# Kernel optimization log

Hardware: AMD Instinct MI355X
Metric: run time of the kernel (lower is better)

The kernel has to match this reference:

```python
import jax, jax.numpy as jnp
import numpy as np

D_MODEL = 1024
N_HEADS = 16
D_K = D_MODEL // N_HEADS


def setup_inputs() -> dict:
    key = jax.random.key(0)
    ks = jax.random.split(key, 9)
    B, S = 4, 2048
    scale = 1.0 / np.sqrt(D_MODEL)
    x = jax.random.normal(ks[0], (B, S, D_MODEL), dtype=jnp.float32)
    # Linear params: weight [out,in] (torch convention), bias [out]
    wq = jax.random.uniform(ks[1], (D_MODEL, D_MODEL), jnp.float32, -scale, scale)
    bq = jax.random.uniform(ks[2], (D_MODEL,), jnp.float32, -scale, scale)
    wk = jax.random.uniform(ks[3], (D_MODEL, D_MODEL), jnp.float32, -scale, scale)
    bk = jax.random.uniform(ks[4], (D_MODEL,), jnp.float32, -scale, scale)
    wv = jax.random.uniform(ks[5], (D_MODEL, D_MODEL), jnp.float32, -scale, scale)
    bv = jax.random.uniform(ks[6], (D_MODEL,), jnp.float32, -scale, scale)
    wo = jax.random.uniform(ks[7], (D_MODEL, D_MODEL), jnp.float32, -scale, scale)
    bo = jax.random.uniform(ks[8], (D_MODEL,), jnp.float32, -scale, scale)
    return {"x": x, "wq": wq, "bq": bq, "wk": wk, "bk": bk,
            "wv": wv, "bv": bv, "wo": wo, "bo": bo}


def reference(x, wq, bq, wk, bk, wv, bv, wo, bo):
    B, S, _ = x.shape
    # QKV projections (torch Linear: x @ W^T + b)
    q = x @ wq.T + bq
    k = x @ wk.T + bk
    v = x @ wv.T + bv
    # [B, H, S, D_K]
    q = q.reshape(B, S, N_HEADS, D_K).transpose(0, 2, 1, 3)
    k = k.reshape(B, S, N_HEADS, D_K).transpose(0, 2, 1, 3)
    v = v.reshape(B, S, N_HEADS, D_K).transpose(0, 2, 1, 3)
    scores = jnp.einsum('bhqd,bhkd->bhqk', q, k) / jnp.sqrt(jnp.float32(D_K))
    attn = jax.nn.softmax(scores, axis=-1)
    out = jnp.einsum('bhqk,bhkd->bhqd', attn, v)
    out = out.transpose(0, 2, 1, 3).reshape(B, S, D_MODEL)
    return out @ wo.T + bo
```

## Files before the change

kernel.cpp:

```cpp
#include <hip/hip_runtime.h>

#define DMODEL 1024
#define NHEADS 16
#define DK 64
#define BATCH 4
#define SEQ 2048
#define MROWS (BATCH * SEQ)
#define NT 16

typedef __attribute__((ext_vector_type(8))) short bf16x8;
typedef __attribute__((ext_vector_type(8))) unsigned short u16x8;
typedef __attribute__((ext_vector_type(4))) unsigned short u16x4;
typedef __attribute__((ext_vector_type(4))) float f32x4;
typedef __attribute__((ext_vector_type(16))) float f32x16;
typedef __attribute__((ext_vector_type(2))) unsigned int u32x2;
typedef __attribute__((ext_vector_type(4))) unsigned int u32x4;

using gld_gptr = const __attribute__((address_space(1))) unsigned int*;
using gld_lptr = __attribute__((address_space(3))) unsigned int*;

#define QSCALE 0.18033688011112042f

__device__ inline unsigned short f32_bf16(float f) {
    unsigned int u = __float_as_uint(f);
    u += 0x7FFFu + ((u >> 16) & 1u);
    return (unsigned short)(u >> 16);
}

__device__ inline unsigned int cvtpk_bf16(float a, float b) {
    unsigned int r;
    asm("v_cvt_pk_bf16_f32 %0, %1, %2" : "=v"(r) : "v"(a), "v"(b));
    return r;
}

__device__ inline f32x16 fz16() {
    f32x16 v;
#pragma unroll
    for (int i = 0; i < 16; ++i) v[i] = 0.f;
    return v;
}

struct Conv5 {
    const float* s[5];
    unsigned short* d[5];
};

__global__ __launch_bounds__(256) void conv5_kernel(Conv5 c) {
    int bx = blockIdx.x;
    int which, idx;
    if (bx < 4096) { which = 0; idx = bx; }
    else { which = 1 + ((bx - 4096) >> 9); idx = (bx - 4096) & 511; }
    int i = idx * 256 + threadIdx.x;
    const float4* s = (const float4*)(c.s[which] + (size_t)i * 8);
    float4 a = s[0], b = s[1];
    u16x8 o;
    o[0] = f32_bf16(a.x); o[1] = f32_bf16(a.y); o[2] = f32_bf16(a.z); o[3] = f32_bf16(a.w);
    o[4] = f32_bf16(b.x); o[5] = f32_bf16(b.y); o[6] = f32_bf16(b.z); o[7] = f32_bf16(b.w);
    *(u16x8*)(c.d[which] + (size_t)i * 8) = o;
}


__device__ __forceinline__ void stage_half(const unsigned short* mat, int row0, int step,
                                           char* lds_half, int tid) {
#pragma unroll
    for (int rnd = 0; rnd < 2; ++rnd) {
        int rl = rnd * 64 + (tid >> 3);
        int c16 = (tid & 7) ^ (rl & 7);
        const unsigned short* g = mat + (size_t)(row0 + rl) * DMODEL + step * 64 + c16 * 8;
        __builtin_amdgcn_global_load_lds((gld_gptr)g,
            (gld_lptr)(lds_half + rnd * 8192 + (tid >> 6) * 1024), 16, 0, 0);
    }
}

__device__ __forceinline__ bf16x8 lds_frag(const char* base, int row, int kk, int l) {
    int kb = kk * 64 + (l >> 4) * 16;
    return *(const bf16x8*)(base + row * 128 + (kb ^ ((row & 7) << 4)));
}

template <int QP>
__device__ __forceinline__ void phase_reads(const char* Ab, const char* Bb,
                                            bf16x8 (&breg)[4][2], bf16x8 (&areg)[2][2],
                                            int wm, int wn, int l) {
    int l15 = l & 15;
    if constexpr (QP == 0) {
#pragma unroll
        for (int nt = 0; nt < 4; ++nt)
#pragma unroll
            for (int kk = 0; kk < 2; ++kk)
                breg[nt][kk] = lds_frag(Bb, wn * 64 + nt * 16 + l15, kk, l);
    }
#pragma unroll
    for (int j = 0; j < 2; ++j)
#pragma unroll
        for (int kk = 0; kk < 2; ++kk)
            areg[j][kk] = lds_frag(Ab, wm * 128 + (QP * 2 + j) * 16 + l15, kk, l);
}

template <int QP>
__device__ __forceinline__ void phase_mfma(bf16x8 (&areg)[2][2], bf16x8 (&breg)[4][2],
                                           f32x4 (&acc)[8][4]) {
    __builtin_amdgcn_s_setprio(1);
#pragma unroll
    for (int j = 0; j < 2; ++j)
#pragma unroll
        for (int nt = 0; nt < 4; ++nt) {
            acc[QP * 2 + j][nt] = __builtin_amdgcn_mfma_f32_16x16x32_bf16(
                areg[j][0], breg[nt][0], acc[QP * 2 + j][nt], 0, 0, 0);
            acc[QP * 2 + j][nt] = __builtin_amdgcn_mfma_f32_16x16x32_bf16(
                areg[j][1], breg[nt][1], acc[QP * 2 + j][nt], 0, 0, 0);
        }
    __builtin_amdgcn_s_setprio(0);
}

#define GBAR() __builtin_amdgcn_s_barrier()
#define VMC4() asm volatile("s_waitcnt vmcnt(4)" ::: "memory")

template <bool F32OUT>
__device__ __forceinline__ void gemm_core(const unsigned short* __restrict__ Am,
                                          const unsigned short* __restrict__ Bm,
                                          const float* __restrict__ bias, void* Cv,
                                          float scl, int m0, int n0) {
    __shared__ __align__(16) char lds[131072];
    char* A0 = lds;
    char* B0 = lds + 32768;
    char* A1 = lds + 65536;
    char* B1 = lds + 98304;

    int tid = threadIdx.x, l = tid & 63, w = tid >> 6;
    int wm = w >> 2, wn = w & 3;

    f32x4 acc[8][4];
#pragma unroll
    for (int i = 0; i < 8; ++i)
#pragma unroll
        for (int j = 0; j < 4; ++j) acc[i][j] = (f32x4){0.f, 0.f, 0.f, 0.f};

    stage_half(Am, m0,       0, A0,         tid);
    stage_half(Am, m0 + 128, 0, A0 + 16384, tid);
    stage_half(Bm, n0,       0, B0,         tid);
    stage_half(Bm, n0 + 128, 0, B0 + 16384, tid);
    stage_half(Bm, n0,       1, B1,         tid);
    stage_half(Bm, n0 + 128, 1, B1 + 16384, tid);
    VMC4();
    GBAR();

    bf16x8 breg[4][2];
    for (int i = 0; i < NT / 2; ++i) {
        int E = 2 * i;
        bf16x8 areg[2][2];
        phase_reads<0>(A0, B0, breg, areg, wm, wn, l);
        stage_half(Am, m0,       (E + 1) & 15, A1, tid);
        GBAR(); phase_mfma<0>(areg, breg, acc); GBAR();

        phase_reads<1>(A0, B0, breg, areg, wm, wn, l);
        stage_half(Am, m0 + 128, (E + 1) & 15, A1 + 16384, tid);
        GBAR(); phase_mfma<1>(areg, breg, acc); GBAR();

        phase_reads<2>(A0, B0, breg, areg, wm, wn, l);
        stage_half(Bm, n0,       (E + 2) & 15, B0, tid);
        GBAR(); phase_mfma<2>(areg, breg, acc); GBAR();

        phase_reads<3>(A0, B0, breg, areg, wm, wn, l);
        stage_half(Bm, n0 + 128, (E + 2) & 15, B0 + 16384, tid);
        GBAR(); phase_mfma<3>(areg, breg, acc);
        VMC4();
        GBAR();

        phase_reads<0>(A1, B1, breg, areg, wm, wn, l);
        stage_half(Am, m0,       (E + 2) & 15, A0, tid);
        GBAR(); phase_mfma<0>(areg, breg, acc); GBAR();

        phase_reads<1>(A1, B1, breg, areg, wm, wn, l);
        stage_half(Am, m0 + 128, (E + 2) & 15, A0 + 16384, tid);
        GBAR(); phase_mfma<1>(areg, breg, acc); GBAR();

        phase_reads<2>(A1, B1, breg, areg, wm, wn, l);
        stage_half(Bm, n0,       (E + 3) & 15, B1, tid);
        GBAR(); phase_mfma<2>(areg, breg, acc); GBAR();

        phase_reads<3>(A1, B1, breg, areg, wm, wn, l);
        stage_half(Bm, n0 + 128, (E + 3) & 15, B1 + 16384, tid);
        GBAR(); phase_mfma<3>(areg, breg, acc);
        VMC4();
        GBAR();
    }

    int lm = l >> 4, ln = l & 15;
#pragma unroll
    for (int nt = 0; nt < 4; ++nt) {
        int col = n0 + wn * 64 + nt * 16 + ln;
        float bv = bias[col];
#pragma unroll
        for (int mt = 0; mt < 8; ++mt)
#pragma unroll
            for (int r = 0; r < 4; ++r) {
                int row = m0 + wm * 128 + mt * 16 + lm * 4 + r;
                float v = (acc[mt][nt][r] + bv) * scl;
                if constexpr (F32OUT)
                    ((float*)Cv)[(size_t)row * DMODEL + col] = v;
                else
                    ((unsigned short*)Cv)[(size_t)row * DMODEL + col] = f32_bf16(v);
            }
    }
}

struct QkvPtrs {
    const unsigned short* w[3];
    const float* b[3];
    unsigned short* c[3];
    float scale[3];
};

__global__ __launch_bounds__(512, 2) void gemm_qkv8(const unsigned short* __restrict__ A, QkvPtrs p) {
    int sel = blockIdx.y >> 2;
    int n0 = (blockIdx.y & 3) * 256;
    int m0 = blockIdx.x * 256;
    gemm_core<false>(A, p.w[sel], p.b[sel], p.c[sel], p.scale[sel], m0, n0);
}

__global__ __launch_bounds__(512, 2) void gemm_out8(const unsigned short* __restrict__ A,
                                                    const unsigned short* __restrict__ B,
                                                    const float* __restrict__ bias,
                                                    float* __restrict__ C) {
    gemm_core<true>(A, B, bias, C, 1.0f, blockIdx.x * 256, blockIdx.y * 256);
}

#define BUILD_PW(dst, pv, o)                                                        \
    {                                                                               \
        unsigned int wa_ = cvtpk_bf16(pv[(o) + 0], pv[(o) + 1]);                    \
        unsigned int wb_ = cvtpk_bf16(pv[(o) + 2], pv[(o) + 3]);                    \
        unsigned int wc_ = cvtpk_bf16(pv[(o) + 4], pv[(o) + 5]);                    \
        unsigned int wd_ = cvtpk_bf16(pv[(o) + 6], pv[(o) + 7]);                    \
        u32x2 ra_ = __builtin_amdgcn_permlane32_swap(wa_, wc_, false, false);       \
        u32x2 rb_ = __builtin_amdgcn_permlane32_swap(wb_, wd_, false, false);       \
        dst = (u32x4){ra_[0], rb_[0], ra_[1], rb_[1]};                              \
    }

__global__ __launch_bounds__(256, 3) void attn_kernel(const unsigned short* __restrict__ Q,
                                                      const unsigned short* __restrict__ Km,
                                                      const unsigned short* __restrict__ Vm,
                                                      unsigned short* __restrict__ O) {
    __shared__ unsigned short Klds[64 * 64];
    __shared__ unsigned short Vt[64 * 64];

    int flat = blockIdx.y * gridDim.x + blockIdx.x;
    int xcd = flat & 7, idx = flat >> 3;
    int bh = xcd * 8 + (idx & 7);
    int qt = idx >> 3;
    int b = bh >> 4, h = bh & 15;
    int tid = threadIdx.x, l = tid & 63, w = tid >> 6;
    int lq = l & 31, hf = l >> 5;
    const size_t base = ((size_t)b * SEQ) * DMODEL + (size_t)h * DK;
    const unsigned short* qp = Q + base;
    const unsigned short* kp = Km + base;
    const unsigned short* vp = Vm + base;
    int qrow = qt * 128 + w * 32 + lq;

    bf16x8 qf[4];
#pragma unroll
    for (int ks = 0; ks < 4; ++ks)
        qf[ks] = *(const bf16x8*)&qp[(size_t)qrow * DMODEL + ks * 16 + hf * 8];

    f32x16 accO[2];
    accO[0] = fz16(); accO[1] = fz16();
    float l_r = 0.f;

    for (int kt = 0; kt < SEQ / 64; ++kt) {
        __syncthreads();
#pragma unroll
        for (int i = 0; i < 2; ++i) {
            int chunk = w + i * 4;
            int row = chunk * 8 + (l >> 3);
            int srccol = (l & 7) ^ (l >> 3);
            const unsigned short* g = kp + (size_t)(kt * 64 + row) * DMODEL + srccol * 8;
            __builtin_amdgcn_global_load_lds((gld_gptr)g, (gld_lptr)(Klds + chunk * 512), 16, 0, 0);
        }
        {
            int kvp = (tid & 31) * 2;
            int d0 = (tid >> 5) * 8;
            bf16x8 va = *(const bf16x8*)&vp[(size_t)(kt * 64 + kvp) * DMODEL + d0];
            bf16x8 vb = *(const bf16x8*)&vp[(size_t)(kt * 64 + kvp + 1) * DMODEL + d0];
#pragma unroll
            for (int j = 0; j < 8; ++j) {
                int d = d0 + j;
                unsigned int val = ((unsigned int)(unsigned short)va[j]) |
                                   (((unsigned int)(unsigned short)vb[j]) << 16);
                int byt = d * 128 + (((kvp >> 3) ^ (d & 7)) << 4) + (kvp & 7) * 2;
                *(unsigned int*)((char*)Vt + byt) = val;
            }
        }
        __syncthreads();

        f32x16 s0 = fz16(), s1 = fz16();
#pragma unroll
        for (int ks = 0; ks < 4; ++ks) {
            int col16 = ks * 2 + hf;
            bf16x8 kf0 = *(const bf16x8*)((const char*)Klds + lq * 128 + ((col16 ^ (lq & 7)) << 4));
            bf16x8 kf1 = *(const bf16x8*)((const char*)Klds + (lq + 32) * 128 + ((col16 ^ (lq & 7)) << 4));
            s0 = __builtin_amdgcn_mfma_f32_32x32x16_bf16(kf0, qf[ks], s0, 0, 0, 0);
            s1 = __builtin_amdgcn_mfma_f32_32x32x16_bf16(kf1, qf[ks], s1, 0, 0, 0);
        }

        float rs = 0.f;
#pragma unroll
        for (int r = 0; r < 16; ++r) { s0[r] = __builtin_amdgcn_exp2f(s0[r]); rs += s0[r]; }
#pragma unroll
        for (int r = 0; r < 16; ++r) { s1[r] = __builtin_amdgcn_exp2f(s1[r]); rs += s1[r]; }
        rs += __shfl_xor(rs, 32);
        l_r += rs;

        u32x4 pw[4];
        BUILD_PW(pw[0], s0, 0);
        BUILD_PW(pw[1], s0, 8);
        BUILD_PW(pw[2], s1, 0);
        BUILD_PW(pw[3], s1, 8);

#pragma unroll
        for (int ks = 0; ks < 4; ++ks) {
            bf16x8 pf = *(bf16x8*)&pw[ks];
            int col16 = ks * 2 + hf;
#pragma unroll
            for (int db = 0; db < 2; ++db) {
                int d = db * 32 + lq;
                bf16x8 vf = *(const bf16x8*)((const char*)Vt + d * 128 + ((col16 ^ (d & 7)) << 4));
                accO[db] = __builtin_amdgcn_mfma_f32_32x32x16_bf16(vf, pf, accO[db], 0, 0, 0);
            }
        }
    }

    float inv = 1.0f / l_r;
    unsigned short* op = O + base + (size_t)qrow * DMODEL;
#pragma unroll
    for (int db = 0; db < 2; ++db)
#pragma unroll
        for (int rg = 0; rg < 4; ++rg) {
            int dbase = db * 32 + rg * 8 + hf * 4;
            u16x4 ov;
#pragma unroll
            for (int j = 0; j < 4; ++j) ov[j] = f32_bf16(accO[db][rg * 4 + j] * inv);
            *(u16x4*)&op[dbase] = ov;
        }
}

extern "C" void kernel_launch(void* const* d_in, const int* in_sizes, int n_in,
                              void* d_out, int out_size, void* d_ws, size_t ws_size,
                              hipStream_t stream) {
    (void)in_sizes; (void)n_in; (void)out_size; (void)ws_size;
    const float* x  = (const float*)d_in[0];
    const float* wq = (const float*)d_in[1];
    const float* bq = (const float*)d_in[2];
    const float* wk = (const float*)d_in[3];
    const float* bk = (const float*)d_in[4];
    const float* wv = (const float*)d_in[5];
    const float* bv = (const float*)d_in[6];
    const float* wo = (const float*)d_in[7];
    const float* bo = (const float*)d_in[8];
    float* out = (float*)d_out;
    char* ws = (char*)d_ws;

    unsigned short* xb  = (unsigned short*)(ws);
    unsigned short* wqb = (unsigned short*)(ws + (16ull << 20));
    unsigned short* wkb = (unsigned short*)(ws + (18ull << 20));
    unsigned short* wvb = (unsigned short*)(ws + (20ull << 20));
    unsigned short* wob = (unsigned short*)(ws + (22ull << 20));
    unsigned short* qb  = (unsigned short*)(ws + (24ull << 20));
    unsigned short* kb  = (unsigned short*)(ws + (40ull << 20));
    unsigned short* vb  = (unsigned short*)(ws + (56ull << 20));
    unsigned short* ob  = xb;

    Conv5 cv;
    cv.s[0] = x;  cv.d[0] = xb;
    cv.s[1] = wq; cv.d[1] = wqb;
    cv.s[2] = wk; cv.d[2] = wkb;
    cv.s[3] = wv; cv.d[3] = wvb;
    cv.s[4] = wo; cv.d[4] = wob;
    conv5_kernel<<<4096 + 4 * 512, 256, 0, stream>>>(cv);

    QkvPtrs p;
    p.w[0] = wqb; p.w[1] = wkb; p.w[2] = wvb;
    p.b[0] = bq;  p.b[1] = bk;  p.b[2] = bv;
    p.c[0] = qb;  p.c[1] = kb;  p.c[2] = vb;
    p.scale[0] = QSCALE; p.scale[1] = 1.0f; p.scale[2] = 1.0f;
    gemm_qkv8<<<dim3(32, 12), 512, 0, stream>>>(xb, p);

    attn_kernel<<<dim3(16, 64), 256, 0, stream>>>(qb, kb, vb, ob);

    gemm_out8<<<dim3(32, 4), 512, 0, stream>>>(ob, wob, bo, out);
}
```

Measured before the change: 200.5 us.

## Double-buffer K/V tiles and double Q rows per wave in attention

The attention kernel now double-buffers the K and V shared-memory tiles, prefetching the next tile while MFMAs run on the current one. This replaces two __syncthreads per tile with a single barrier. Each wave now handles 64 query rows instead of 32, so every K/V fragment read from LDS feeds twice as many MFMAs, and the grid is halved to match. The changes also add s_setprio around the MFMA blocks and lower launch bounds occupancy to 2, trading occupancy and more registers for better reuse and latency hiding.

Result: faster. 188.9 us (-5.8%).

```diff
diff --git a/kernel.cpp b/kernel.cpp
--- a/kernel.cpp
+++ b/kernel.cpp
@@ -59,7 +59,6 @@
     *(u16x8*)(c.d[which] + (size_t)i * 8) = o;
 }
 
-
 __device__ __forceinline__ void stage_half(const unsigned short* mat, int row0, int step,
                                            char* lds_half, int tid) {
 #pragma unroll
@@ -236,12 +235,47 @@
         dst = (u32x4){ra_[0], rb_[0], ra_[1], rb_[1]};                              \
     }
 
-__global__ __launch_bounds__(256, 3) void attn_kernel(const unsigned short* __restrict__ Q,
+#define ABAR() asm volatile("s_barrier" ::: "memory")
+#define AVMC0() asm volatile("s_waitcnt vmcnt(0)" ::: "memory")
+
+__device__ __forceinline__ void stage_k(const unsigned short* kp, int kt,
+                                        unsigned short* kbuf, int l, int w) {
+#pragma unroll
+    for (int i = 0; i < 2; ++i) {
+        int chunk = w + i * 4;
+        int srccol = (l & 7) ^ (l >> 3);
+        const unsigned short* g = kp + (size_t)(kt * 64 + chunk * 8 + (l >> 3)) * DMODEL + srccol * 8;
+        __builtin_amdgcn_global_load_lds((gld_gptr)g, (gld_lptr)(kbuf + chunk * 512), 16, 0, 0);
+    }
+}
+
+__device__ __forceinline__ void load_v(const unsigned short* vp, int kt, int tid,
+                                       bf16x8& va, bf16x8& vb) {
+    int kvp = (tid & 31) * 2;
+    int d0 = (tid >> 5) * 8;
+    va = *(const bf16x8*)&vp[(size_t)(kt * 64 + kvp) * DMODEL + d0];
+    vb = *(const bf16x8*)&vp[(size_t)(kt * 64 + kvp + 1) * DMODEL + d0];
+}
+
+__device__ __forceinline__ void write_v(unsigned short* vbuf, int tid, bf16x8 va, bf16x8 vb) {
+    int kvp = (tid & 31) * 2;
+    int d0 = (tid >> 5) * 8;
+#pragma unroll
+    for (int j = 0; j < 8; ++j) {
+        int d = d0 + j;
+        unsigned int val = ((unsigned int)(unsigned short)va[j]) |
+                           (((unsigned int)(unsigned short)vb[j]) << 16);
+        int byt = d * 128 + (((kvp >> 3) ^ (d & 7)) << 4) + (kvp & 7) * 2;
+        *(unsigned int*)((char*)vbuf + byt) = val;
+    }
+}
+
+__global__ __launch_bounds__(256, 2) void attn_kernel(const unsigned short* __restrict__ Q,
                                                       const unsigned short* __restrict__ Km,
                                                       const unsigned short* __restrict__ Vm,
                                                       unsigned short* __restrict__ O) {
-    __shared__ unsigned short Klds[64 * 64];
-    __shared__ unsigned short Vt[64 * 64];
+    __shared__ unsigned short Klds[2][64 * 64];
+    __shared__ unsigned short Vt[2][64 * 64];
 
     int flat = blockIdx.y * gridDim.x + blockIdx.x;
     int xcd = flat & 7, idx = flat >> 3;
@@ -254,92 +288,103 @@
     const unsigned short* qp = Q + base;
     const unsigned short* kp = Km + base;
     const unsigned short* vp = Vm + base;
-    int qrow = qt * 128 + w * 32 + lq;
-
-    bf16x8 qf[4];
-#pragma unroll
-    for (int ks = 0; ks < 4; ++ks)
-        qf[ks] = *(const bf16x8*)&qp[(size_t)qrow * DMODEL + ks * 16 + hf * 8];
-
-    f32x16 accO[2];
-    accO[0] = fz16(); accO[1] = fz16();
-    float l_r = 0.f;
+    int q0 = qt * 256 + w * 64;
+
+    bf16x8 qf[2][4];
+#pragma unroll
+    for (int sb = 0; sb < 2; ++sb)
+#pragma unroll
+        for (int ks = 0; ks < 4; ++ks)
+            qf[sb][ks] = *(const bf16x8*)&qp[(size_t)(q0 + sb * 32 + lq) * DMODEL + ks * 16 + hf * 8];
+
+    f32x16 accO[2][2];
+    accO[0][0] = fz16(); accO[0][1] = fz16(); accO[1][0] = fz16(); accO[1][1] = fz16();
+    float l_r[2] = {0.f, 0.f};
+
+    bf16x8 va, vb;
+    stage_k(kp, 0, Klds[0], l, w);
+    load_v(vp, 0, tid, va, vb);
+    AVMC0();
+    write_v(Vt[0], tid, va, vb);
+    ABAR();
 
     for (int kt = 0; kt < SEQ / 64; ++kt) {
-        __syncthreads();
-#pragma unroll
-        for (int i = 0; i < 2; ++i) {
-            int chunk = w + i * 4;
-            int row = chunk * 8 + (l >> 3);
-            int srccol = (l & 7) ^ (l >> 3);
-            const unsigned short* g = kp + (size_t)(kt * 64 + row) * DMODEL + srccol * 8;
-            __builtin_amdgcn_global_load_lds((gld_gptr)g, (gld_lptr)(Klds + chunk * 512), 16, 0, 0);
-        }
-        {
-            int kvp = (tid & 31) * 2;
-            int d0 = (tid >> 5) * 8;
-            bf16x8 va = *(const bf16x8*)&vp[(size_t)(kt * 64 + kvp) * DMODEL + d0];
-            bf16x8 vb = *(const bf16x8*)&vp[(size_t)(kt * 64 + kvp + 1) * DMODEL + d0];
-#pragma unroll
-            for (int j = 0; j < 8; ++j) {
-                int d = d0 + j;
-                unsigned int val = ((unsigned int)(unsigned short)va[j]) |
-                                   (((unsigned int)(unsigned short)vb[j]) << 16);
-                int byt = d * 128 + (((kvp >> 3) ^ (d & 7)) << 4) + (kvp & 7) * 2;
-                *(unsigned int*)((char*)Vt + byt) = val;
-            }
-        }
-        __syncthreads();
-
-        f32x16 s0 = fz16(), s1 = fz16();
+        int cur = kt & 1, nxt = cur ^ 1;
+        bool pre = (kt + 1 < SEQ / 64);
+        if (pre) {
+            stage_k(kp, kt + 1, Klds[nxt], l, w);
+            load_v(vp, kt + 1, tid, va, vb);
+        }
+
+        f32x16 s[2][2];
+        s[0][0] = fz16(); s[0][1] = fz16(); s[1][0] = fz16(); s[1][1] = fz16();
+        __builtin_amdgcn_s_setprio(1);
 #pragma unroll
         for (int ks = 0; ks < 4; ++ks) {
             int col16 = ks * 2 + hf;
-            bf16x8 kf0 = *(const bf16x8*)((const char*)Klds + lq * 128 + ((col16 ^ (lq & 7)) << 4));
-            bf16x8 kf1 = *(const bf16x8*)((const char*)Klds + (lq + 32) * 128 + ((col16 ^ (lq & 7)) << 4));
-            s0 = __builtin_amdgcn_mfma_f32_32x32x16_bf16(kf0, qf[ks], s0, 0, 0, 0);
-            s1 = __builtin_amdgcn_mfma_f32_32x32x16_bf16(kf1, qf[ks], s1, 0, 0, 0);
-        }
-
-        float rs = 0.f;
-#pragma unroll
-        for (int r = 0; r < 16; ++r) { s0[r] = __builtin_amdgcn_exp2f(s0[r]); rs += s0[r]; }
-#pragma unroll
-        for (int r = 0; r < 16; ++r) { s1[r] = __builtin_amdgcn_exp2f(s1[r]); rs += s1[r]; }
-        rs += __shfl_xor(rs, 32);
-        l_r += rs;
-
-        u32x4 pw[4];
-        BUILD_PW(pw[0], s0, 0);
-        BUILD_PW(pw[1], s0, 8);
-        BUILD_PW(pw[2], s1, 0);
-        BUILD_PW(pw[3], s1, 8);
-
+            bf16x8 kf0 = *(const bf16x8*)((const char*)Klds[cur] + lq * 128 + ((col16 ^ (lq & 7)) << 4));
+            bf16x8 kf1 = *(const bf16x8*)((const char*)Klds[cur] + (lq + 32) * 128 + ((col16 ^ (lq & 7)) << 4));
+            s[0][0] = __builtin_amdgcn_mfma_f32_32x32x16_bf16(kf0, qf[0][ks], s[0][0], 0, 0, 0);
+            s[0][1] = __builtin_amdgcn_mfma_f32_32x32x16_bf16(kf1, qf[0][ks], s[0][1], 0, 0, 0);
+            s[1][0] = __builtin_amdgcn_mfma_f32_32x32x16_bf16(kf0, qf[1][ks], s[1][0], 0, 0, 0);
+            s[1][1] = __builtin_amdgcn_mfma_f32_32x32x16_bf16(kf1, qf[1][ks], s[1][1], 0, 0, 0);
+        }
+        __builtin_amdgcn_s_setprio(0);
+
+        u32x4 pw[2][4];
+#pragma unroll
+        for (int sb = 0; sb < 2; ++sb) {
+            float rs = 0.f;
+#pragma unroll
+            for (int r = 0; r < 16; ++r) { s[sb][0][r] = __builtin_amdgcn_exp2f(s[sb][0][r]); rs += s[sb][0][r]; }
+#pragma unroll
+            for (int r = 0; r < 16; ++r) { s[sb][1][r] = __builtin_amdgcn_exp2f(s[sb][1][r]); rs += s[sb][1][r]; }
+            rs += __shfl_xor(rs, 32);
+            l_r[sb] += rs;
+            BUILD_PW(pw[sb][0], s[sb][0], 0);
+            BUILD_PW(pw[sb][1], s[sb][0], 8);
+            BUILD_PW(pw[sb][2], s[sb][1], 0);
+            BUILD_PW(pw[sb][3], s[sb][1], 8);
+        }
+
+        __builtin_amdgcn_s_setprio(1);
 #pragma unroll
         for (int ks = 0; ks < 4; ++ks) {
-            bf16x8 pf = *(bf16x8*)&pw[ks];
             int col16 = ks * 2 + hf;
-#pragma unroll
-            for (int db = 0; db < 2; ++db) {
-                int d = db * 32 + lq;
-                bf16x8 vf = *(const bf16x8*)((const char*)Vt + d * 128 + ((col16 ^ (d & 7)) << 4));
-                accO[db] = __builtin_amdgcn_mfma_f32_32x32x16_bf16(vf, pf, accO[db], 0, 0, 0);
+            int d1 = 32 + lq;
+            bf16x8 vf0 = *(const bf16x8*)((const char*)Vt[cur] + lq * 128 + ((col16 ^ (lq & 7)) << 4));
+            bf16x8 vf1 = *(const bf16x8*)((const char*)Vt[cur] + d1 * 128 + ((col16 ^ (d1 & 7)) << 4));
+            bf16x8 pf0 = *(bf16x8*)&pw[0][ks];
+            bf16x8 pf1 = *(bf16x8*)&pw[1][ks];
+            accO[0][0] = __builtin_amdgcn_mfma_f32_32x32x16_bf16(vf0, pf0, accO[0][0], 0, 0, 0);
+            accO[0][1] = __builtin_amdgcn_mfma_f32_32x32x16_bf16(vf1, pf0, accO[0][1], 0, 0, 0);
+            accO[1][0] = __builtin_amdgcn_mfma_f32_32x32x16_bf16(vf0, pf1, accO[1][0], 0, 0, 0);
+            accO[1][1] = __builtin_amdgcn_mfma_f32_32x32x16_bf16(vf1, pf1, accO[1][1], 0, 0, 0);
+        }
+        __builtin_amdgcn_s_setprio(0);
+
+        if (pre) {
+            AVMC0();
+            write_v(Vt[nxt], tid, va, vb);
+        }
+        ABAR();
+    }
+
+#pragma unroll
+    for (int sb = 0; sb < 2; ++sb) {
+        float inv = 1.0f / l_r[sb];
+        unsigned short* op = O + base + (size_t)(q0 + sb * 32 + lq) * DMODEL;
+#pragma unroll
+        for (int db = 0; db < 2; ++db)
+#pragma unroll
+            for (int rg = 0; rg < 4; ++rg) {
+                int dbase = db * 32 + rg * 8 + hf * 4;
+                u16x4 ov;
+#pragma unroll
+                for (int j = 0; j < 4; ++j) ov[j] = f32_bf16(accO[sb][db][rg * 4 + j] * inv);
+                *(u16x4*)&op[dbase] = ov;
             }
-        }
-    }
-
-    float inv = 1.0f / l_r;
-    unsigned short* op = O + base + (size_t)qrow * DMODEL;
-#pragma unroll
-    for (int db = 0; db < 2; ++db)
-#pragma unroll
-        for (int rg = 0; rg < 4; ++rg) {
-            int dbase = db * 32 + rg * 8 + hf * 4;
-            u16x4 ov;
-#pragma unroll
-            for (int j = 0; j < 4; ++j) ov[j] = f32_bf16(accO[db][rg * 4 + j] * inv);
-            *(u16x4*)&op[dbase] = ov;
-        }
+    }
 }
 
 extern "C" void kernel_launch(void* const* d_in, const int* in_sizes, int n_in,
@@ -383,7 +428,7 @@
     p.scale[0] = QSCALE; p.scale[1] = 1.0f; p.scale[2] = 1.0f;
     gemm_qkv8<<<dim3(32, 12), 512, 0, stream>>>(xb, p);
 
-    attn_kernel<<<dim3(16, 64), 256, 0, stream>>>(qb, kb, vb, ob);
+    attn_kernel<<<dim3(8, 64), 256, 0, stream>>>(qb, kb, vb, ob);
 
     gemm_out8<<<dim3(32, 4), 512, 0, stream>>>(ob, wob, bo, out);
 }
```
